# Kernel tuning notes

Hardware: AMD Instinct MI355X
Metric: run time of the kernel (lower is better)

The kernel has to match this reference:

```python
import jax, jax.numpy as jnp
import numpy as np

B, D, H, C, V, SAMPLE_NUM = 4096, 1024, 512, 50, 4, 10000


def ds_combin_two(alpha1, alpha2, K):
    """Dempster-Shafer combination of two Dirichlet parameter sets [B, K]."""
    S1 = jnp.sum(alpha1, axis=1, keepdims=True)
    S2 = jnp.sum(alpha2, axis=1, keepdims=True)
    b1 = (alpha1 - 1.0) / S1
    b2 = (alpha2 - 1.0) / S2
    u1 = K / S1  # [B,1]
    u2 = K / S2
    # bb_sum - bb_diag computed without materializing [B,K,K] outer product:
    # sum_ij b1_i b2_j = sum(b1)*sum(b2); diag sum = sum_i b1_i b2_i
    Cconf = jnp.sum(b1, axis=1) * jnp.sum(b2, axis=1) - jnp.sum(b1 * b2, axis=1)  # [B]
    denom = (1.0 - Cconf)[:, None]
    b_a = (b1 * b2 + b1 * u2 + b2 * u1) / denom
    u_a = (u1 * u2) / denom  # [B,1]
    S_a = K / u_a
    e_a = b_a * S_a
    return e_a + 1.0


def setup_inputs() -> dict:
    key = jax.random.key(0)
    ks = jax.random.split(key, 8)
    x = jax.random.normal(ks[0], (V, B, D), dtype=jnp.float32)
    indexes = jax.random.randint(ks[1], (B,), 0, SAMPLE_NUM)
    W1 = jax.random.normal(ks[2], (V, D, H), dtype=jnp.float32) * (1.0 / np.sqrt(D))
    b1 = jax.random.normal(ks[3], (V, H), dtype=jnp.float32) * 0.01
    W2 = jax.random.normal(ks[4], (V, H, C), dtype=jnp.float32) * (1.0 / np.sqrt(H))
    b2 = jax.random.normal(ks[5], (V, C), dtype=jnp.float32) * 0.01
    # original init: identity per (view, sample); add small noise so the
    eye = jnp.eye(C, dtype=jnp.float32)
    matrixes = eye[None, None] + 0.01 * jax.random.normal(ks[6], (V, SAMPLE_NUM, C, C), dtype=jnp.float32)
    return {"x": x, "indexes": indexes, "W1": W1, "b1": b1, "W2": W2, "b2": b2, "matrixes": matrixes}


def reference(x, indexes, W1, b1, W2, b2, matrixes):
    K = W2.shape[-1]
    n_views = x.shape[0]
    # per-view classifier MLP: Linear->ReLU->Linear->Softplus
    h = jax.nn.relu(jnp.einsum("vbd,vdh->vbh", x, W1) + b1[:, None, :])
    evidence = jax.nn.softplus(jnp.einsum("vbh,vhc->vbc", h, W2) + b2[:, None, :])  # [V,B,C]
    # transferByMatrix (training path): per-sample gathered [C,C] matmul
    sel = matrixes[:, indexes]  # [V,B,C,C]
    transferred = jnp.einsum("vbc,vbcd->vbd", evidence, sel)  # [V,B,C]
    t_alpha = transferred + 1.0
    # sequential DS combination over views
    alpha_a = t_alpha[0]
    for v in range(1, n_views):
        alpha_a = ds_combin_two(alpha_a, t_alpha[v], K)
    evidence_a = alpha_a - 1.0  # [B,C]
    return transferred, evidence_a, evidence
```

## Files before the change

kernel.cpp:

```cpp
#include <hip/hip_runtime.h>
#include <hip/hip_bf16.h>
#include <math.h>

typedef unsigned short u16;
typedef __attribute__((ext_vector_type(8))) short bf16x8;
typedef __attribute__((ext_vector_type(4))) float f32x4;

#define DEVI __device__ __forceinline__

constexpr int NV = 4;
constexpr int NB = 4096;
constexpr int ND = 1024;
constexpr int NH = 512;
constexpr int NC = 50;
constexpr int NSAMP = 10000;
constexpr int NCP = 64;

DEVI u16 to_bf16(float f) {
  union { float f; unsigned u; } v; v.f = f;
  unsigned r = v.u + 0x7fffu + ((v.u >> 16) & 1u);
  return (u16)(r >> 16);
}

DEVI u16 cvt_bf16(float f) {
  __hip_bfloat16 h = __float2bfloat16(f);
  return *reinterpret_cast<u16*>(&h);
}

DEVI float wsum(float x) {
#pragma unroll
  for (int m = 32; m > 0; m >>= 1) x += __shfl_xor(x, m, 64);
  return x;
}

#define GLD_LDS16(gsrc, ldst)                                                  \
  __builtin_amdgcn_global_load_lds(                                            \
      (const __attribute__((address_space(1))) void*)(gsrc),                   \
      (__attribute__((address_space(3))) void*)(ldst), 16, 0, 0)

__global__ __launch_bounds__(256) void k_transpose_w1(const float* __restrict__ W1,
                                                      u16* __restrict__ W1T) {
  __shared__ float tile[32][33];
  const int v = blockIdx.z;
  const int d0 = blockIdx.x * 32;
  const int h0 = blockIdx.y * 32;
  const float* src = W1 + (size_t)v * ND * NH;
  u16* dst = W1T + (size_t)v * NH * ND;
  const int tx = threadIdx.x, ty = threadIdx.y;
#pragma unroll
  for (int j = 0; j < 32; j += 8)
    tile[ty + j][tx] = src[(size_t)(d0 + ty + j) * NH + h0 + tx];
  __syncthreads();
#pragma unroll
  for (int j = 0; j < 32; j += 8)
    dst[(size_t)(h0 + ty + j) * ND + d0 + tx] = to_bf16(tile[tx][ty + j]);
}

__global__ __launch_bounds__(256) void k_prep_w2(const float* __restrict__ W2,
                                                 u16* __restrict__ W2T) {
  int i = blockIdx.x * blockDim.x + threadIdx.x;
  if (i >= NV * NCP * NH) return;
  int h = i % NH;
  int c = (i / NH) % NCP;
  int v = i / (NCP * NH);
  float val = (c < NC) ? W2[((size_t)v * NH + h) * NC + c] : 0.f;
  W2T[i] = to_bf16(val);
}

__global__ __launch_bounds__(256) void k_gemm1(const float* __restrict__ Xf,
                                               const u16* __restrict__ W1T,
                                               const float* __restrict__ b1,
                                               u16* __restrict__ Hb) {
  constexpr int BM = 128, BN = 128, BK = 32;
  const int v = blockIdx.z;
  const int m0 = blockIdx.x * BM;
  const int n0 = blockIdx.y * BN;
  __shared__ u16 As[BM][BK];
  __shared__ u16 Bs[BN][BK];
  const float* Ag = Xf + (size_t)v * NB * ND + (size_t)m0 * ND;
  const u16* Bg = W1T + (size_t)v * NH * ND + (size_t)n0 * ND;
  const int tid = threadIdx.x;
  const int lane = tid & 63;
  const int wv = tid >> 6;
  const int wr = wv >> 1, wc = wv & 1;
  const int rA = tid >> 3;
  const int cA = (tid & 7) * 4;
  const int rB = tid >> 2;
  const int cB = (tid & 3) * 8;

  f32x4 acc[4][4] = {};

  float4 pa[4];
#pragma unroll
  for (int i = 0; i < 4; ++i)
    pa[i] = *(const float4*)(Ag + (size_t)(rA + i * 32) * ND + cA);

  for (int k0 = 0; k0 < ND; k0 += BK) {
    __syncthreads();
#pragma unroll
    for (int i = 0; i < 4; ++i) {
      ushort4 u;
      u.x = cvt_bf16(pa[i].x); u.y = cvt_bf16(pa[i].y);
      u.z = cvt_bf16(pa[i].z); u.w = cvt_bf16(pa[i].w);
      *(ushort4*)&As[rA + i * 32][cA] = u;
    }
    GLD_LDS16(Bg + (size_t)rB * ND + k0 + cB,        &Bs[rB][cB]);
    GLD_LDS16(Bg + (size_t)(rB + 64) * ND + k0 + cB, &Bs[rB + 64][cB]);
    __syncthreads();

    if (k0 + BK < ND) {
#pragma unroll
      for (int i = 0; i < 4; ++i)
        pa[i] = *(const float4*)(Ag + (size_t)(rA + i * 32) * ND + k0 + BK + cA);
    }

    const int fr = lane & 15;
    const int kb = (lane >> 4) * 8;
    bf16x8 af[4], bf[4];
#pragma unroll
    for (int mi = 0; mi < 4; ++mi)
      af[mi] = *(const bf16x8*)&As[wr * 64 + mi * 16 + fr][kb];
#pragma unroll
    for (int ni = 0; ni < 4; ++ni)
      bf[ni] = *(const bf16x8*)&Bs[wc * 64 + ni * 16 + fr][kb];
#pragma unroll
    for (int mi = 0; mi < 4; ++mi)
#pragma unroll
      for (int ni = 0; ni < 4; ++ni)
        acc[mi][ni] = __builtin_amdgcn_mfma_f32_16x16x32_bf16(
            af[mi], bf[ni], acc[mi][ni], 0, 0, 0);
  }

  const int frow = (lane >> 4) * 4;
  const int fcol = lane & 15;
#pragma unroll
  for (int mi = 0; mi < 4; ++mi) {
#pragma unroll
    for (int ni = 0; ni < 4; ++ni) {
      const int n = n0 + wc * 64 + ni * 16 + fcol;
      const float bias = b1[v * NH + n];
#pragma unroll
      for (int j = 0; j < 4; ++j) {
        const int m = m0 + wr * 64 + mi * 16 + frow + j;
        float val = fmaxf(acc[mi][ni][j] + bias, 0.f);
        Hb[(size_t)v * NB * NH + (size_t)m * NH + n] = to_bf16(val);
      }
    }
  }
}

__global__ __launch_bounds__(256) void k_gemm2(const u16* __restrict__ Hb,
                                               const u16* __restrict__ W2T,
                                               const float* __restrict__ b2,
                                               float* __restrict__ out_ev) {
  constexpr int BM = 64, BK = 32;
  const int v = blockIdx.z;
  const int m0 = blockIdx.x * BM;
  __shared__ u16 As[BM][BK];
  __shared__ u16 Bs[NCP][BK];
  const u16* Ag = Hb + (size_t)v * NB * NH + (size_t)m0 * NH;
  const u16* Bg = W2T + (size_t)v * NCP * NH;
  const int tid = threadIdx.x;
  const int lane = tid & 63;
  const int wv = tid >> 6;
  const int r = tid >> 2;
  const int c8 = (tid & 3) * 8;

  f32x4 acc[4] = {};

  for (int k0 = 0; k0 < NH; k0 += BK) {
    __syncthreads();
    GLD_LDS16(Ag + (size_t)r * NH + k0 + c8, &As[r][c8]);
    GLD_LDS16(Bg + (size_t)r * NH + k0 + c8, &Bs[r][c8]);
    __syncthreads();

    const int fr = lane & 15;
    const int kb = (lane >> 4) * 8;
    bf16x8 af = *(const bf16x8*)&As[wv * 16 + fr][kb];
#pragma unroll
    for (int ni = 0; ni < 4; ++ni) {
      bf16x8 bf = *(const bf16x8*)&Bs[ni * 16 + fr][kb];
      acc[ni] = __builtin_amdgcn_mfma_f32_16x16x32_bf16(af, bf, acc[ni], 0, 0, 0);
    }
  }

  const int frow = (lane >> 4) * 4;
  const int fcol = lane & 15;
#pragma unroll
  for (int ni = 0; ni < 4; ++ni) {
    const int n = ni * 16 + fcol;
    if (n < NC) {
      const float bias = b2[v * NC + n];
#pragma unroll
      for (int j = 0; j < 4; ++j) {
        const int m = m0 + wv * 16 + frow + j;
        float x = acc[ni][j] + bias;
        float sp = fmaxf(x, 0.f) + log1pf(expf(-fabsf(x)));
        out_ev[(size_t)v * NB * NC + (size_t)m * NC + n] = sp;
      }
    }
  }
}

__global__ __launch_bounds__(256) void k_tc(const float* __restrict__ evf,
                                            const float* __restrict__ mats,
                                            const int* __restrict__ idx,
                                            float* __restrict__ out_tr,
                                            float* __restrict__ out_ea) {
  const int b = blockIdx.x * 4 + (threadIdx.x >> 6);
  const int lane = threadIdx.x & 63;
  if (b >= NB) return;
  const bool act = lane < NC;
  const float Kf = (float)NC;
  const int ix = idx[b];

  float ta[NV];
#pragma unroll
  for (int v = 0; v < NV; ++v) {
    float acc = 0.f;
    if (act) {
      const float* e = evf + ((size_t)v * NB + b) * NC;
      const float* M = mats + ((size_t)v * NSAMP + ix) * NC * NC;
#pragma unroll
      for (int c = 0; c < NC; ++c)
        acc = fmaf(e[c], M[c * NC + lane], acc);
      out_tr[((size_t)v * NB + b) * NC + lane] = acc;
    }
    ta[v] = act ? acc + 1.0f : 0.0f;
  }

  float alpha = ta[0];
#pragma unroll
  for (int v = 1; v < NV; ++v) {
    float a2 = ta[v];
    float S1 = wsum(act ? alpha : 0.f);
    float S2 = wsum(act ? a2 : 0.f);
    float b1v = act ? (alpha - 1.f) / S1 : 0.f;
    float b2v = act ? (a2 - 1.f) / S2 : 0.f;
    float u1 = Kf / S1, u2 = Kf / S2;
    float sb1 = wsum(b1v);
    float sb2 = wsum(b2v);
    float sb12 = wsum(b1v * b2v);
    float Cconf = sb1 * sb2 - sb12;
    float denom = 1.f - Cconf;
    float b_a = (b1v * b2v + b1v * u2 + b2v * u1) / denom;
    float u_a = u1 * u2 / denom;
    float S_a = Kf / u_a;
    alpha = b_a * S_a + 1.f;
  }
  if (act) out_ea[(size_t)b * NC + lane] = alpha - 1.f;
}

extern "C" void kernel_launch(void* const* d_in, const int* in_sizes, int n_in,
                              void* d_out, int out_size, void* d_ws, size_t ws_size,
                              hipStream_t stream) {
  const float *x = nullptr, *W1 = nullptr, *b1 = nullptr, *W2 = nullptr,
              *b2 = nullptr, *mats = nullptr;
  const int* idx = nullptr;
  for (int i = 0; i < n_in; ++i) {
    switch (in_sizes[i]) {
      case 16777216:  x    = (const float*)d_in[i]; break;
      case 4096:      idx  = (const int*)d_in[i];   break;
      case 2097152:   W1   = (const float*)d_in[i]; break;
      case 2048:      b1   = (const float*)d_in[i]; break;
      case 102400:    W2   = (const float*)d_in[i]; break;
      case 200:       b2   = (const float*)d_in[i]; break;
      case 100000000: mats = (const float*)d_in[i]; break;
      default: break;
    }
  }
  if (!x || !idx || !W1 || !b1 || !W2 || !b2 || !mats) return;

  char* ws = (char*)d_ws;
  u16* w1t = (u16*)(ws + 0);
  u16* w2t = (u16*)(ws + 4194304);
  u16* hb  = (u16*)(ws + 4456448);

  float* out_tr = (float*)d_out;
  float* out_ea = out_tr + (size_t)NV * NB * NC;
  float* out_ev = out_ea + (size_t)NB * NC;

  k_transpose_w1<<<dim3(ND / 32, NH / 32, NV), dim3(32, 8), 0, stream>>>(W1, w1t);
  k_prep_w2<<<(NV * NCP * NH + 255) / 256, 256, 0, stream>>>(W2, w2t);
  k_gemm1<<<dim3(NB / 128, NH / 128, NV), 256, 0, stream>>>(x, w1t, b1, hb);
  k_gemm2<<<dim3(NB / 64, 1, NV), 256, 0, stream>>>(hb, w2t, b2, out_ev);
  k_tc<<<NB / 4, 256, 0, stream>>>(out_ev, mats, idx, out_tr, out_ea);
}
```

Before: 92.36 us.

## Double-buffer LDS tiles in both GEMM kernels to overlap loads with MFMA

Both GEMM kernels switch to double-buffered shared-memory tiles. The next K-slice is loaded into the alternate buffer while MFMAs run on the current one, so each iteration needs one barrier instead of two. This is meant to hide global-to-LDS latency behind compute, at the cost of twice the LDS footprint, which could lower occupancy.

```diff
diff --git a/kernel.cpp b/kernel.cpp
--- a/kernel.cpp
+++ b/kernel.cpp
@@ -75,8 +75,8 @@
   const int v = blockIdx.z;
   const int m0 = blockIdx.x * BM;
   const int n0 = blockIdx.y * BN;
-  __shared__ u16 As[BM][BK];
-  __shared__ u16 Bs[BN][BK];
+  __shared__ u16 As[2][BM][BK];
+  __shared__ u16 Bs[2][BN][BK];
   const float* Ag = Xf + (size_t)v * NB * ND + (size_t)m0 * ND;
   const u16* Bg = W1T + (size_t)v * NH * ND + (size_t)n0 * ND;
   const int tid = threadIdx.x;
@@ -89,46 +89,60 @@
   const int cB = (tid & 3) * 8;
 
   f32x4 acc[4][4] = {};
-
   float4 pa[4];
+
 #pragma unroll
   for (int i = 0; i < 4; ++i)
     pa[i] = *(const float4*)(Ag + (size_t)(rA + i * 32) * ND + cA);
+  GLD_LDS16(Bg + (size_t)rB * ND + cB,        &Bs[0][rB][cB]);
+  GLD_LDS16(Bg + (size_t)(rB + 64) * ND + cB, &Bs[0][rB + 64][cB]);
+#pragma unroll
+  for (int i = 0; i < 4; ++i) {
+    ushort4 u;
+    u.x = cvt_bf16(pa[i].x); u.y = cvt_bf16(pa[i].y);
+    u.z = cvt_bf16(pa[i].z); u.w = cvt_bf16(pa[i].w);
+    *(ushort4*)&As[0][rA + i * 32][cA] = u;
+  }
+#pragma unroll
+  for (int i = 0; i < 4; ++i)
+    pa[i] = *(const float4*)(Ag + (size_t)(rA + i * 32) * ND + BK + cA);
+  __syncthreads();
 
   for (int k0 = 0; k0 < ND; k0 += BK) {
-    __syncthreads();
-#pragma unroll
-    for (int i = 0; i < 4; ++i) {
-      ushort4 u;
-      u.x = cvt_bf16(pa[i].x); u.y = cvt_bf16(pa[i].y);
-      u.z = cvt_bf16(pa[i].z); u.w = cvt_bf16(pa[i].w);
-      *(ushort4*)&As[rA + i * 32][cA] = u;
-    }
-    GLD_LDS16(Bg + (size_t)rB * ND + k0 + cB,        &Bs[rB][cB]);
-    GLD_LDS16(Bg + (size_t)(rB + 64) * ND + k0 + cB, &Bs[rB + 64][cB]);
-    __syncthreads();
-
+    const int cur = (k0 >> 5) & 1;
+    const int nxt = cur ^ 1;
     if (k0 + BK < ND) {
-#pragma unroll
-      for (int i = 0; i < 4; ++i)
-        pa[i] = *(const float4*)(Ag + (size_t)(rA + i * 32) * ND + k0 + BK + cA);
-    }
-
+      GLD_LDS16(Bg + (size_t)rB * ND + k0 + BK + cB,        &Bs[nxt][rB][cB]);
+      GLD_LDS16(Bg + (size_t)(rB + 64) * ND + k0 + BK + cB, &Bs[nxt][rB + 64][cB]);
+#pragma unroll
+      for (int i = 0; i < 4; ++i) {
+        ushort4 u;
+        u.x = cvt_bf16(pa[i].x); u.y = cvt_bf16(pa[i].y);
+        u.z = cvt_bf16(pa[i].z); u.w = cvt_bf16(pa[i].w);
+        *(ushort4*)&As[nxt][rA + i * 32][cA] = u;
+      }
+      if (k0 + 2 * BK < ND) {
+#pragma unroll
+        for (int i = 0; i < 4; ++i)
+          pa[i] = *(const float4*)(Ag + (size_t)(rA + i * 32) * ND + k0 + 2 * BK + cA);
+      }
+    }
     const int fr = lane & 15;
     const int kb = (lane >> 4) * 8;
     bf16x8 af[4], bf[4];
 #pragma unroll
     for (int mi = 0; mi < 4; ++mi)
-      af[mi] = *(const bf16x8*)&As[wr * 64 + mi * 16 + fr][kb];
+      af[mi] = *(const bf16x8*)&As[cur][wr * 64 + mi * 16 + fr][kb];
 #pragma unroll
     for (int ni = 0; ni < 4; ++ni)
-      bf[ni] = *(const bf16x8*)&Bs[wc * 64 + ni * 16 + fr][kb];
+      bf[ni] = *(const bf16x8*)&Bs[cur][wc * 64 + ni * 16 + fr][kb];
 #pragma unroll
     for (int mi = 0; mi < 4; ++mi)
 #pragma unroll
       for (int ni = 0; ni < 4; ++ni)
         acc[mi][ni] = __builtin_amdgcn_mfma_f32_16x16x32_bf16(
             af[mi], bf[ni], acc[mi][ni], 0, 0, 0);
+    __syncthreads();
   }
 
   const int frow = (lane >> 4) * 4;
@@ -156,8 +170,8 @@
   constexpr int BM = 64, BK = 32;
   const int v = blockIdx.z;
   const int m0 = blockIdx.x * BM;
-  __shared__ u16 As[BM][BK];
-  __shared__ u16 Bs[NCP][BK];
+  __shared__ u16 As[2][BM][BK];
+  __shared__ u16 Bs[2][NCP][BK];
   const u16* Ag = Hb + (size_t)v * NB * NH + (size_t)m0 * NH;
   const u16* Bg = W2T + (size_t)v * NCP * NH;
   const int tid = threadIdx.x;
@@ -168,20 +182,26 @@
 
   f32x4 acc[4] = {};
 
+  GLD_LDS16(Ag + (size_t)r * NH + c8, &As[0][r][c8]);
+  GLD_LDS16(Bg + (size_t)r * NH + c8, &Bs[0][r][c8]);
+  __syncthreads();
+
   for (int k0 = 0; k0 < NH; k0 += BK) {
-    __syncthreads();
-    GLD_LDS16(Ag + (size_t)r * NH + k0 + c8, &As[r][c8]);
-    GLD_LDS16(Bg + (size_t)r * NH + k0 + c8, &Bs[r][c8]);
-    __syncthreads();
-
+    const int cur = (k0 >> 5) & 1;
+    const int nxt = cur ^ 1;
+    if (k0 + BK < NH) {
+      GLD_LDS16(Ag + (size_t)r * NH + k0 + BK + c8, &As[nxt][r][c8]);
+      GLD_LDS16(Bg + (size_t)r * NH + k0 + BK + c8, &Bs[nxt][r][c8]);
+    }
     const int fr = lane & 15;
     const int kb = (lane >> 4) * 8;
-    bf16x8 af = *(const bf16x8*)&As[wv * 16 + fr][kb];
+    bf16x8 af = *(const bf16x8*)&As[cur][wv * 16 + fr][kb];
 #pragma unroll
     for (int ni = 0; ni < 4; ++ni) {
-      bf16x8 bf = *(const bf16x8*)&Bs[ni * 16 + fr][kb];
+      bf16x8 bf = *(const bf16x8*)&Bs[cur][ni * 16 + fr][kb];
       acc[ni] = __builtin_amdgcn_mfma_f32_16x16x32_bf16(af, bf, acc[ni], 0, 0, 0);
     }
+    __syncthreads();
   }
 
   const int frow = (lane >> 4) * 4;
```

Measured after the change: 93.70 us. Within noise of the previous version (+1.5%).

## Restructure transfer kernel: one block per sample, wave per view, LDS-staged matrices

Applied to the files above, without the earlier changes.

The transfer/DS kernel now uses one block per sample with one wavefront per view instead of one wavefront handling all four views serially. Each wave stages its gathered 50x50 matrix into LDS using direct global-to-LDS loads, then computes its view's transfer from LDS. Results go through shared memory to wave 0, which runs the sequential DS combination. The aim is more memory-level parallelism on the gathered matrix reads, at the cost of 4x more blocks, about 41KB of LDS per block, two block barriers, and three waves idle during the combination.

```diff
diff --git a/kernel.cpp b/kernel.cpp
--- a/kernel.cpp
+++ b/kernel.cpp
@@ -207,48 +207,63 @@
                                             const int* __restrict__ idx,
                                             float* __restrict__ out_tr,
                                             float* __restrict__ out_ea) {
-  const int b = blockIdx.x * 4 + (threadIdx.x >> 6);
+  __shared__ float Mlds[NV][2560];
+  __shared__ float taLds[NV][64];
+  const int b = blockIdx.x;
+  const int v = threadIdx.x >> 6;
   const int lane = threadIdx.x & 63;
-  if (b >= NB) return;
   const bool act = lane < NC;
   const float Kf = (float)NC;
   const int ix = idx[b];
 
-  float ta[NV];
-#pragma unroll
-  for (int v = 0; v < NV; ++v) {
-    float acc = 0.f;
-    if (act) {
-      const float* e = evf + ((size_t)v * NB + b) * NC;
-      const float* M = mats + ((size_t)v * NSAMP + ix) * NC * NC;
-#pragma unroll
-      for (int c = 0; c < NC; ++c)
-        acc = fmaf(e[c], M[c * NC + lane], acc);
-      out_tr[((size_t)v * NB + b) * NC + lane] = acc;
-    }
-    ta[v] = act ? acc + 1.0f : 0.0f;
-  }
-
-  float alpha = ta[0];
-#pragma unroll
-  for (int v = 1; v < NV; ++v) {
-    float a2 = ta[v];
-    float S1 = wsum(act ? alpha : 0.f);
-    float S2 = wsum(act ? a2 : 0.f);
-    float b1v = act ? (alpha - 1.f) / S1 : 0.f;
-    float b2v = act ? (a2 - 1.f) / S2 : 0.f;
-    float u1 = Kf / S1, u2 = Kf / S2;
-    float sb1 = wsum(b1v);
-    float sb2 = wsum(b2v);
-    float sb12 = wsum(b1v * b2v);
-    float Cconf = sb1 * sb2 - sb12;
-    float denom = 1.f - Cconf;
-    float b_a = (b1v * b2v + b1v * u2 + b2v * u1) / denom;
-    float u_a = u1 * u2 / denom;
-    float S_a = Kf / u_a;
-    alpha = b_a * S_a + 1.f;
-  }
-  if (act) out_ea[(size_t)b * NC + lane] = alpha - 1.f;
+  const float* Mg = mats + ((size_t)v * NSAMP + ix) * NC * NC;
+#pragma unroll
+  for (int it = 0; it < 9; ++it)
+    GLD_LDS16(Mg + (size_t)(it * 64 + lane) * 4, &Mlds[v][(it * 64 + lane) * 4]);
+  if (lane < 49) {
+    float4 t = *(const float4*)(Mg + (size_t)(576 + lane) * 4);
+    *(float4*)&Mlds[v][(576 + lane) * 4] = t;
+  }
+  __syncthreads();
+
+  const float* e = evf + ((size_t)v * NB + b) * NC;
+  float acc = 0.f;
+  if (act) {
+#pragma unroll
+    for (int c = 0; c < NC; ++c)
+      acc = fmaf(e[c], Mlds[v][c * NC + lane], acc);
+    out_tr[((size_t)v * NB + b) * NC + lane] = acc;
+  }
+  taLds[v][lane] = acc;
+  __syncthreads();
+
+  if (v == 0) {
+    float ta[NV];
+#pragma unroll
+    for (int vv = 0; vv < NV; ++vv)
+      ta[vv] = act ? taLds[vv][lane] + 1.0f : 0.0f;
+
+    float alpha = ta[0];
+#pragma unroll
+    for (int vv = 1; vv < NV; ++vv) {
+      float a2 = ta[vv];
+      float S1 = wsum(act ? alpha : 0.f);
+      float S2 = wsum(act ? a2 : 0.f);
+      float b1v = act ? (alpha - 1.f) / S1 : 0.f;
+      float b2v = act ? (a2 - 1.f) / S2 : 0.f;
+      float u1 = Kf / S1, u2 = Kf / S2;
+      float sb1 = wsum(b1v);
+      float sb2 = wsum(b2v);
+      float sb12 = wsum(b1v * b2v);
+      float Cconf = sb1 * sb2 - sb12;
+      float denom = 1.f - Cconf;
+      float b_a = (b1v * b2v + b1v * u2 + b2v * u1) / denom;
+      float u_a = u1 * u2 / denom;
+      float S_a = Kf / u_a;
+      alpha = b_a * S_a + 1.f;
+    }
+    if (act) out_ea[(size_t)b * NC + lane] = alpha - 1.f;
+  }
 }
 
 extern "C" void kernel_launch(void* const* d_in, const int* in_sizes, int n_in,
@@ -284,5 +299,5 @@
   k_prep_w2<<<(NV * NCP * NH + 255) / 256, 256, 0, stream>>>(W2, w2t);
   k_gemm1<<<dim3(NB / 128, NH / 128, NV), 256, 0, stream>>>(x, w1t, b1, hb);
   k_gemm2<<<dim3(NB / 64, 1, NV), 256, 0, stream>>>(hb, w2t, b2, out_ev);
-  k_tc<<<NB / 4, 256, 0, stream>>>(out_ev, mats, idx, out_tr, out_ea);
-}
+  k_tc<<<NB, 256, 0, stream>>>(out_ev, mats, idx, out_tr, out_ea);
+}
```

New measurement: 99.58 us. 1.08x slower.

## Load GEMM fragments directly from global into registers, drop LDS staging

Applied to the files above, without the earlier changes.

Both GEMM kernels stop staging A/B tiles through shared memory with barriers. Each wave now loads its MFMA fragments directly from global memory into registers, double-buffered across K steps, and converts X to bf16 in registers. This removes LDS traffic and __syncthreads, but duplicates global loads across waves sharing the same rows or columns and relies on cache hits for reuse.

```diff
diff --git a/kernel.cpp b/kernel.cpp
--- a/kernel.cpp
+++ b/kernel.cpp
@@ -27,16 +27,20 @@
   return *reinterpret_cast<u16*>(&h);
 }
 
+DEVI bf16x8 cvt8(float4 a, float4 b) {
+  bf16x8 r;
+  r[0] = (short)cvt_bf16(a.x); r[1] = (short)cvt_bf16(a.y);
+  r[2] = (short)cvt_bf16(a.z); r[3] = (short)cvt_bf16(a.w);
+  r[4] = (short)cvt_bf16(b.x); r[5] = (short)cvt_bf16(b.y);
+  r[6] = (short)cvt_bf16(b.z); r[7] = (short)cvt_bf16(b.w);
+  return r;
+}
+
 DEVI float wsum(float x) {
 #pragma unroll
   for (int m = 32; m > 0; m >>= 1) x += __shfl_xor(x, m, 64);
   return x;
 }
-
-#define GLD_LDS16(gsrc, ldst)                                                  \
-  __builtin_amdgcn_global_load_lds(                                            \
-      (const __attribute__((address_space(1))) void*)(gsrc),                   \
-      (__attribute__((address_space(3))) void*)(ldst), 16, 0, 0)
 
 __global__ __launch_bounds__(256) void k_transpose_w1(const float* __restrict__ W1,
                                                       u16* __restrict__ W1T) {
@@ -75,60 +79,52 @@
   const int v = blockIdx.z;
   const int m0 = blockIdx.x * BM;
   const int n0 = blockIdx.y * BN;
-  __shared__ u16 As[BM][BK];
-  __shared__ u16 Bs[BN][BK];
-  const float* Ag = Xf + (size_t)v * NB * ND + (size_t)m0 * ND;
-  const u16* Bg = W1T + (size_t)v * NH * ND + (size_t)n0 * ND;
   const int tid = threadIdx.x;
   const int lane = tid & 63;
   const int wv = tid >> 6;
   const int wr = wv >> 1, wc = wv & 1;
-  const int rA = tid >> 3;
-  const int cA = (tid & 7) * 4;
-  const int rB = tid >> 2;
-  const int cB = (tid & 3) * 8;
+  const int fr = lane & 15;
+  const int kb = (lane >> 4) * 8;
+
+  const float* A0 = Xf + (size_t)v * NB * ND + (size_t)(m0 + wr * 64 + fr) * ND + kb;
+  const u16*   B0 = W1T + (size_t)v * NH * ND + (size_t)(n0 + wc * 64 + fr) * ND + kb;
 
   f32x4 acc[4][4] = {};
-
-  float4 pa[4];
-#pragma unroll
-  for (int i = 0; i < 4; ++i)
-    pa[i] = *(const float4*)(Ag + (size_t)(rA + i * 32) * ND + cA);
-
-  for (int k0 = 0; k0 < ND; k0 += BK) {
-    __syncthreads();
-#pragma unroll
-    for (int i = 0; i < 4; ++i) {
-      ushort4 u;
-      u.x = cvt_bf16(pa[i].x); u.y = cvt_bf16(pa[i].y);
-      u.z = cvt_bf16(pa[i].z); u.w = cvt_bf16(pa[i].w);
-      *(ushort4*)&As[rA + i * 32][cA] = u;
-    }
-    GLD_LDS16(Bg + (size_t)rB * ND + k0 + cB,        &Bs[rB][cB]);
-    GLD_LDS16(Bg + (size_t)(rB + 64) * ND + k0 + cB, &Bs[rB + 64][cB]);
-    __syncthreads();
-
-    if (k0 + BK < ND) {
-#pragma unroll
-      for (int i = 0; i < 4; ++i)
-        pa[i] = *(const float4*)(Ag + (size_t)(rA + i * 32) * ND + k0 + BK + cA);
-    }
-
-    const int fr = lane & 15;
-    const int kb = (lane >> 4) * 8;
-    bf16x8 af[4], bf[4];
-#pragma unroll
-    for (int mi = 0; mi < 4; ++mi)
-      af[mi] = *(const bf16x8*)&As[wr * 64 + mi * 16 + fr][kb];
+  float4 pa0[8], pa1[8];
+  bf16x8 pb0[4], pb1[4];
+
+  auto LA = [&](float4* pa, int k) {
+#pragma unroll
+    for (int mi = 0; mi < 4; ++mi) {
+      const float* p = A0 + (size_t)mi * 16 * ND + k;
+      pa[2 * mi]     = *(const float4*)p;
+      pa[2 * mi + 1] = *(const float4*)(p + 4);
+    }
+  };
+  auto LB = [&](bf16x8* pb, int k) {
 #pragma unroll
     for (int ni = 0; ni < 4; ++ni)
-      bf[ni] = *(const bf16x8*)&Bs[wc * 64 + ni * 16 + fr][kb];
+      pb[ni] = *(const bf16x8*)(B0 + (size_t)ni * 16 * ND + k);
+  };
+  auto CMP = [&](const float4* pa, const bf16x8* pb) {
+    bf16x8 af[4];
+#pragma unroll
+    for (int mi = 0; mi < 4; ++mi) af[mi] = cvt8(pa[2 * mi], pa[2 * mi + 1]);
 #pragma unroll
     for (int mi = 0; mi < 4; ++mi)
 #pragma unroll
       for (int ni = 0; ni < 4; ++ni)
         acc[mi][ni] = __builtin_amdgcn_mfma_f32_16x16x32_bf16(
-            af[mi], bf[ni], acc[mi][ni], 0, 0, 0);
+            af[mi], pb[ni], acc[mi][ni], 0, 0, 0);
+  };
+
+  LA(pa0, 0);
+  LB(pb0, 0);
+  for (int k0 = 0; k0 < ND; k0 += 2 * BK) {
+    if (k0 + BK < ND) { LA(pa1, k0 + BK); LB(pb1, k0 + BK); }
+    CMP(pa0, pb0);
+    if (k0 + 2 * BK < ND) { LA(pa0, k0 + 2 * BK); LB(pb0, k0 + 2 * BK); }
+    if (k0 + BK < ND) CMP(pa1, pb1);
   }
 
   const int frow = (lane >> 4) * 4;
@@ -156,32 +152,37 @@
   constexpr int BM = 64, BK = 32;
   const int v = blockIdx.z;
   const int m0 = blockIdx.x * BM;
-  __shared__ u16 As[BM][BK];
-  __shared__ u16 Bs[NCP][BK];
-  const u16* Ag = Hb + (size_t)v * NB * NH + (size_t)m0 * NH;
-  const u16* Bg = W2T + (size_t)v * NCP * NH;
   const int tid = threadIdx.x;
   const int lane = tid & 63;
   const int wv = tid >> 6;
-  const int r = tid >> 2;
-  const int c8 = (tid & 3) * 8;
+  const int fr = lane & 15;
+  const int kb = (lane >> 4) * 8;
+
+  const u16* A0 = Hb + (size_t)v * NB * NH + (size_t)(m0 + wv * 16 + fr) * NH + kb;
+  const u16* B0 = W2T + (size_t)v * NCP * NH + (size_t)fr * NH + kb;
 
   f32x4 acc[4] = {};
-
-  for (int k0 = 0; k0 < NH; k0 += BK) {
-    __syncthreads();
-    GLD_LDS16(Ag + (size_t)r * NH + k0 + c8, &As[r][c8]);
-    GLD_LDS16(Bg + (size_t)r * NH + k0 + c8, &Bs[r][c8]);
-    __syncthreads();
-
-    const int fr = lane & 15;
-    const int kb = (lane >> 4) * 8;
-    bf16x8 af = *(const bf16x8*)&As[wv * 16 + fr][kb];
-#pragma unroll
-    for (int ni = 0; ni < 4; ++ni) {
-      bf16x8 bf = *(const bf16x8*)&Bs[ni * 16 + fr][kb];
-      acc[ni] = __builtin_amdgcn_mfma_f32_16x16x32_bf16(af, bf, acc[ni], 0, 0, 0);
-    }
+  bf16x8 a0, a1, b0_[4], b1_[4];
+
+  auto LA = [&](bf16x8& a, int k) { a = *(const bf16x8*)(A0 + k); };
+  auto LB = [&](bf16x8* b, int k) {
+#pragma unroll
+    for (int ni = 0; ni < 4; ++ni)
+      b[ni] = *(const bf16x8*)(B0 + (size_t)ni * 16 * NH + k);
+  };
+  auto CMP = [&](bf16x8 a, const bf16x8* b) {
+#pragma unroll
+    for (int ni = 0; ni < 4; ++ni)
+      acc[ni] = __builtin_amdgcn_mfma_f32_16x16x32_bf16(a, b[ni], acc[ni], 0, 0, 0);
+  };
+
+  LA(a0, 0);
+  LB(b0_, 0);
+  for (int k0 = 0; k0 < NH; k0 += 2 * BK) {
+    if (k0 + BK < NH) { LA(a1, k0 + BK); LB(b1_, k0 + BK); }
+    CMP(a0, b0_);
+    if (k0 + 2 * BK < NH) { LA(a0, k0 + 2 * BK); LB(b0_, k0 + 2 * BK); }
+    if (k0 + BK < NH) CMP(a1, b1_);
   }
 
   const int frow = (lane >> 4) * 4;
```

Result: slower. 147.3 us (+59.5%).
